# Optimization experiments

Hardware: AMD Instinct MI355X
Metric: run time of the kernel (lower is better)

## Reference

```python
import jax, jax.numpy as jnp
import numpy as np

B, N, D, C, E, K = 8, 8192, 128, 128, 8, 2


def setup_inputs() -> dict:
    key = jax.random.key(0)
    k0, k1, k2 = jax.random.split(key, 3)
    x = jax.random.normal(k0, (B, N, D), dtype=jnp.float32)
    router_w = jax.random.normal(k1, (D, E), dtype=jnp.float32) * 0.05
    router_b = jnp.zeros((E,), dtype=jnp.float32)
    expert_w = jax.random.normal(k2, (E, D, C), dtype=jnp.float32) * (1.0 / np.sqrt(D))
    expert_b = jnp.zeros((E, C), dtype=jnp.float32)
    return {"x": x, "router_w": router_w, "router_b": router_b,
            "expert_w": expert_w, "expert_b": expert_b}


def reference(x, router_w, router_b, expert_w, expert_b):
    # Router: softmax over experts, then top-k gating with renormalization.
    router_probs = jax.nn.softmax(x @ router_w + router_b, axis=-1)      # [B,N,E]
    top_p, top_i = jax.lax.top_k(router_probs, K)                        # [B,N,K]
    top_p = top_p / jnp.sum(top_p, axis=-1, keepdims=True)
    # Naive all-expert dense compute (faithful to original): [B,N,E,C]
    expert_out = jnp.einsum('bnd,edc->bnec', x, expert_w) + expert_b
    # Gather the K selected experts per token: [B,N,K,C]
    gathered = jnp.take_along_axis(expert_out, top_i[..., None], axis=2)
    # Weighted combine over selected experts: [B,N,C]
    return jnp.einsum('bnk,bnkc->bnc', top_p, gathered)
```

## Files before the change

### kernel.cpp

```cpp
#include <hip/hip_runtime.h>
#include <hip/hip_bf16.h>
#include <stdint.h>

#define Dd 128
#define Cc 128
#define Ee 8
#define TM 64
#define NTOK 65536

using f32x4  = __attribute__((ext_vector_type(4))) float;
using short8 = __attribute__((ext_vector_type(8))) short;
typedef unsigned short u16;

__device__ inline u16 f2bf(float f) {
    union { __hip_bfloat16 h; u16 u; } cv;
    cv.h = __float2bfloat16(f);
    return cv.u;
}

__global__ __launch_bounds__(256) void transpose_w(const float* __restrict__ w,
                                                   u16* __restrict__ wt) {
    int id = blockIdx.x * 256 + threadIdx.x;
    int cc = id & 15;
    int c  = (id >> 4) & 127;
    int e  = id >> 11;
    const float* src = w + (e << 14) + (cc << 3) * Dd + c;
    u16 tmp[8];
    #pragma unroll
    for (int k = 0; k < 8; ++k) tmp[k] = f2bf(src[k * Dd]);
    int slot = cc ^ (c & 7);
    *(int4*)&wt[(e << 14) + (c << 7) + (slot << 3)] = *(const int4*)tmp;
}

__global__ __launch_bounds__(256, 2) void moe_main(
    const float* __restrict__ x,
    const float* __restrict__ rw,
    const float* __restrict__ rb,
    const float* __restrict__ eb,
    const u16*   __restrict__ wt,
    float*       __restrict__ out)
{
    __shared__ __align__(16) u16 Ws[2][Cc * Dd];
    __shared__ float glg[TM * Ee];

    const int tid  = threadIdx.x;
    const int t0   = blockIdx.x * TM;
    const int lane = tid & 63;
    const int wave = tid >> 6;
    const int m0   = (wave >> 1) * 32;
    const int n0   = (wave & 1) * 64;
    const int ln15 = lane & 15;
    const int kg   = lane >> 4;

    int4 rstg[8];
    {
        const int4* src = (const int4*)wt;
        #pragma unroll
        for (int j = 0; j < 8; ++j) rstg[j] = src[j * 256 + tid];
    }

    {
        int p  = tid * 2;
        int tk = p >> 3, e0 = p & 7;
        const float4* xr = (const float4*)(x + (size_t)(t0 + tk) * Dd);
        double a0 = (double)rb[e0], a1 = (double)rb[e0 + 1];
        #pragma unroll 8
        for (int q = 0; q < 32; ++q) {
            float4 v = xr[q];
            #pragma unroll
            for (int u = 0; u < 4; ++u) {
                double xv = (double)((const float*)&v)[u];
                a0 += xv * (double)rw[(q * 4 + u) * Ee + e0];
                a1 += xv * (double)rw[(q * 4 + u) * Ee + e0 + 1];
            }
        }
        glg[p] = (float)a0;
        glg[p + 1] = (float)a1;
    }

    short8 af[2][4];
    #pragma unroll
    for (int mi = 0; mi < 2; ++mi) {
        int r = t0 + m0 + mi * 16 + ln15;
        #pragma unroll
        for (int ks = 0; ks < 4; ++ks) {
            const float4* s = (const float4*)(x + (size_t)r * Dd + (ks * 4 + kg) * 8);
            float4 a = s[0], b = s[1];
            short8 v;
            v[0] = (short)f2bf(a.x); v[1] = (short)f2bf(a.y);
            v[2] = (short)f2bf(a.z); v[3] = (short)f2bf(a.w);
            v[4] = (short)f2bf(b.x); v[5] = (short)f2bf(b.y);
            v[6] = (short)f2bf(b.z); v[7] = (short)f2bf(b.w);
            af[mi][ks] = v;
        }
    }

    {
        int4* dst = (int4*)Ws[0];
        #pragma unroll
        for (int j = 0; j < 8; ++j) dst[j * 256 + tid] = rstg[j];
    }
    __syncthreads();

    if (tid < TM) {
        float l[Ee];
        #pragma unroll
        for (int k = 0; k < Ee; ++k) l[k] = glg[tid * Ee + k];
        int e0 = 0;
        #pragma unroll
        for (int k = 1; k < Ee; ++k) if (l[k] > l[e0]) e0 = k;
        int e1 = (e0 == 0) ? 1 : 0;
        #pragma unroll
        for (int k = 0; k < Ee; ++k)
            if (k != e0 && l[k] > l[e1]) e1 = k;
        float g1 = __expf(l[e1] - l[e0]);
        float s  = 1.0f + g1;
        float g0 = 1.0f / s; g1 = g1 / s;
        #pragma unroll
        for (int k = 0; k < Ee; ++k) glg[tid * Ee + k] = 0.0f;
        glg[tid * Ee + e0] = g0;
        glg[tid * Ee + e1] = g1;
    }

    f32x4 oacc[2][4] = {};

    for (int e = 0; e < Ee; ++e) {
        if (e < Ee - 1) {
            const int4* src = (const int4*)(wt + ((size_t)(e + 1) << 14));
            #pragma unroll
            for (int j = 0; j < 8; ++j) rstg[j] = src[j * 256 + tid];
        }

        const u16* wsc = Ws[e & 1];
        f32x4 acc[2][4] = {};
        #pragma unroll
        for (int ks = 0; ks < 4; ++ks) {
            short8 bfr[4];
            int cc = ks * 4 + kg;
            #pragma unroll
            for (int ni = 0; ni < 4; ++ni) {
                int r = n0 + ni * 16 + ln15;
                bfr[ni] = *(const short8*)&wsc[r * Dd + ((cc ^ (r & 7)) << 3)];
            }
            #pragma unroll
            for (int mi = 0; mi < 2; ++mi)
                #pragma unroll
                for (int ni = 0; ni < 4; ++ni)
                    acc[mi][ni] = __builtin_amdgcn_mfma_f32_16x16x32_bf16(
                        af[mi][ks], bfr[ni], acc[mi][ni], 0, 0, 0);
        }

        if (e < Ee - 1) {
            int4* dst = (int4*)Ws[(e + 1) & 1];
            #pragma unroll
            for (int j = 0; j < 8; ++j) dst[j * 256 + tid] = rstg[j];
        }
        __syncthreads();

        float bb[4];
        #pragma unroll
        for (int ni = 0; ni < 4; ++ni) bb[ni] = eb[e * Cc + n0 + ni * 16 + ln15];
        #pragma unroll
        for (int mi = 0; mi < 2; ++mi)
            #pragma unroll
            for (int r = 0; r < 4; ++r) {
                float g = glg[(m0 + mi * 16 + kg * 4 + r) * Ee + e];
                #pragma unroll
                for (int ni = 0; ni < 4; ++ni)
                    oacc[mi][ni][r] += g * (acc[mi][ni][r] + bb[ni]);
            }
    }

    #pragma unroll
    for (int mi = 0; mi < 2; ++mi)
        #pragma unroll
        for (int r = 0; r < 4; ++r) {
            size_t row = (size_t)(t0 + m0 + mi * 16 + kg * 4 + r);
            #pragma unroll
            for (int ni = 0; ni < 4; ++ni)
                out[row * Cc + n0 + ni * 16 + ln15] = oacc[mi][ni][r];
        }
}

extern "C" void kernel_launch(void* const* d_in, const int* in_sizes, int n_in,
                              void* d_out, int out_size, void* d_ws, size_t ws_size,
                              hipStream_t stream) {
    const float* x  = (const float*)d_in[0];
    const float* rw = (const float*)d_in[1];
    const float* rb = (const float*)d_in[2];
    const float* ew = (const float*)d_in[3];
    const float* eb = (const float*)d_in[4];
    float* out = (float*)d_out;
    u16* wt = (u16*)d_ws;

    transpose_w<<<dim3(64), dim3(256), 0, stream>>>(ew, wt);
    moe_main<<<dim3(NTOK / TM), dim3(256), 0, stream>>>(x, rw, rb, eb, wt, out);
}
```

Before: 136.8 us.

## Double token tile to 128 with 512-thread blocks and smem-staged weight transpose

```diff
diff --git a/kernel.cpp b/kernel.cpp
--- a/kernel.cpp
+++ b/kernel.cpp
@@ -5,8 +5,10 @@
 #define Dd 128
 #define Cc 128
 #define Ee 8
-#define TM 64
+#define TM 128
+#define NTHR 512
 #define NTOK 65536
+#define GSTR 9
 
 using f32x4  = __attribute__((ext_vector_type(4))) float;
 using short8 = __attribute__((ext_vector_type(8))) short;
@@ -20,19 +22,33 @@
 
 __global__ __launch_bounds__(256) void transpose_w(const float* __restrict__ w,
                                                    u16* __restrict__ wt) {
-    int id = blockIdx.x * 256 + threadIdx.x;
-    int cc = id & 15;
-    int c  = (id >> 4) & 127;
-    int e  = id >> 11;
-    const float* src = w + (e << 14) + (cc << 3) * Dd + c;
-    u16 tmp[8];
-    #pragma unroll
-    for (int k = 0; k < 8; ++k) tmp[k] = f2bf(src[k * Dd]);
-    int slot = cc ^ (c & 7);
-    *(int4*)&wt[(e << 14) + (c << 7) + (slot << 3)] = *(const int4*)tmp;
-}
-
-__global__ __launch_bounds__(256, 2) void moe_main(
+    __shared__ u16 T[16][132];
+    int e    = blockIdx.x >> 3;
+    int dblk = blockIdx.x & 7;
+    int tid  = threadIdx.x;
+    {
+        int dl = tid >> 7;
+        int c  = tid & 127;
+        const float* src = w + (e << 14) + ((dblk * 16) << 7) + c;
+        #pragma unroll
+        for (int i = 0; i < 8; ++i) {
+            int d = i * 2 + dl;
+            T[d][c] = f2bf(src[d << 7]);
+        }
+    }
+    __syncthreads();
+    {
+        int c2 = tid >> 1, j = tid & 1;
+        int cc = dblk * 2 + j;
+        u16 tmp[8];
+        #pragma unroll
+        for (int k = 0; k < 8; ++k) tmp[k] = T[j * 8 + k][c2];
+        int slot = cc ^ (c2 & 7);
+        *(int4*)&wt[(e << 14) + (c2 << 7) + (slot << 3)] = *(const int4*)tmp;
+    }
+}
+
+__global__ __launch_bounds__(NTHR, 4) void moe_main(
     const float* __restrict__ x,
     const float* __restrict__ rw,
     const float* __restrict__ rb,
@@ -41,7 +57,7 @@
     float*       __restrict__ out)
 {
     __shared__ __align__(16) u16 Ws[2][Cc * Dd];
-    __shared__ float glg[TM * Ee];
+    __shared__ float glg[TM * GSTR];
 
     const int tid  = threadIdx.x;
     const int t0   = blockIdx.x * TM;
@@ -52,11 +68,11 @@
     const int ln15 = lane & 15;
     const int kg   = lane >> 4;
 
-    int4 rstg[8];
+    int4 rstg[4];
     {
         const int4* src = (const int4*)wt;
         #pragma unroll
-        for (int j = 0; j < 8; ++j) rstg[j] = src[j * 256 + tid];
+        for (int j = 0; j < 4; ++j) rstg[j] = src[j * NTHR + tid];
     }
 
     {
@@ -74,8 +90,8 @@
                 a1 += xv * (double)rw[(q * 4 + u) * Ee + e0 + 1];
             }
         }
-        glg[p] = (float)a0;
-        glg[p + 1] = (float)a1;
+        glg[tk * GSTR + e0]     = (float)a0;
+        glg[tk * GSTR + e0 + 1] = (float)a1;
     }
 
     short8 af[2][4];
@@ -98,14 +114,14 @@
     {
         int4* dst = (int4*)Ws[0];
         #pragma unroll
-        for (int j = 0; j < 8; ++j) dst[j * 256 + tid] = rstg[j];
+        for (int j = 0; j < 4; ++j) dst[j * NTHR + tid] = rstg[j];
     }
     __syncthreads();
 
     if (tid < TM) {
         float l[Ee];
         #pragma unroll
-        for (int k = 0; k < Ee; ++k) l[k] = glg[tid * Ee + k];
+        for (int k = 0; k < Ee; ++k) l[k] = glg[tid * GSTR + k];
         int e0 = 0;
         #pragma unroll
         for (int k = 1; k < Ee; ++k) if (l[k] > l[e0]) e0 = k;
@@ -117,9 +133,9 @@
         float s  = 1.0f + g1;
         float g0 = 1.0f / s; g1 = g1 / s;
         #pragma unroll
-        for (int k = 0; k < Ee; ++k) glg[tid * Ee + k] = 0.0f;
-        glg[tid * Ee + e0] = g0;
-        glg[tid * Ee + e1] = g1;
+        for (int k = 0; k < Ee; ++k) glg[tid * GSTR + k] = 0.0f;
+        glg[tid * GSTR + e0] = g0;
+        glg[tid * GSTR + e1] = g1;
     }
 
     f32x4 oacc[2][4] = {};
@@ -128,7 +144,7 @@
         if (e < Ee - 1) {
             const int4* src = (const int4*)(wt + ((size_t)(e + 1) << 14));
             #pragma unroll
-            for (int j = 0; j < 8; ++j) rstg[j] = src[j * 256 + tid];
+            for (int j = 0; j < 4; ++j) rstg[j] = src[j * NTHR + tid];
         }
 
         const u16* wsc = Ws[e & 1];
@@ -153,7 +169,7 @@
         if (e < Ee - 1) {
             int4* dst = (int4*)Ws[(e + 1) & 1];
             #pragma unroll
-            for (int j = 0; j < 8; ++j) dst[j * 256 + tid] = rstg[j];
+            for (int j = 0; j < 4; ++j) dst[j * NTHR + tid] = rstg[j];
         }
         __syncthreads();
 
@@ -164,7 +180,7 @@
         for (int mi = 0; mi < 2; ++mi)
             #pragma unroll
             for (int r = 0; r < 4; ++r) {
-                float g = glg[(m0 + mi * 16 + kg * 4 + r) * Ee + e];
+                float g = glg[(m0 + mi * 16 + kg * 4 + r) * GSTR + e];
                 #pragma unroll
                 for (int ni = 0; ni < 4; ++ni)
                     oacc[mi][ni][r] += g * (acc[mi][ni][r] + bb[ni]);
@@ -194,5 +210,5 @@
     u16* wt = (u16*)d_ws;
 
     transpose_w<<<dim3(64), dim3(256), 0, stream>>>(ew, wt);
-    moe_main<<<dim3(NTOK / TM), dim3(256), 0, stream>>>(x, rw, rb, eb, wt, out);
-}
+    moe_main<<<dim3(NTOK / TM), dim3(NTHR), 0, stream>>>(x, rw, rb, eb, wt, out);
+}
```

Result: slower. 146.2 us (+6.8%).
